# Kernel tuning notes

Measured on AMD Instinct MI355X. Metric: run time of the kernel, lower is better.

Reference implementation:

```python
import jax, jax.numpy as jnp
import numpy as np

VOCAB = 50257
EMB = 256
HID = 256
B = 128
S = 2048


def setup_inputs() -> dict:
    key = jax.random.key(0)
    ks = jax.random.split(key, 18)
    w = 0.05  # weight scale to keep tanh/sigmoid in a sane range
    return {
        "x": jax.random.randint(ks[0], (B,), 0, VOCAB),
        "encoder_states": jax.random.normal(ks[1], (S, B, HID), jnp.float32),
        "hidden": jax.random.normal(ks[2], (1, B, HID), jnp.float32),
        "cell": jax.random.normal(ks[3], (1, B, HID), jnp.float32),
        "emb_table": jax.random.normal(ks[4], (VOCAB, EMB), jnp.float32) * w,
        "W_ih": jax.random.normal(ks[5], (4 * HID, EMB + HID), jnp.float32) * w,
        "W_hh": jax.random.normal(ks[6], (4 * HID, HID), jnp.float32) * w,
        "b_ih": jax.random.normal(ks[7], (4 * HID,), jnp.float32) * w,
        "b_hh": jax.random.normal(ks[8], (4 * HID,), jnp.float32) * w,
        "fc_w": jax.random.normal(ks[9], (VOCAB, HID), jnp.float32) * w,
        "fc_b": jax.random.normal(ks[10], (VOCAB,), jnp.float32) * w,
        "W1_w": jax.random.normal(ks[11], (HID, HID), jnp.float32) * w,
        "W1_b": jax.random.normal(ks[12], (HID,), jnp.float32) * w,
        "W2_w": jax.random.normal(ks[13], (HID, HID), jnp.float32) * w,
        "W2_b": jax.random.normal(ks[14], (HID,), jnp.float32) * w,
        "V_w": jax.random.normal(ks[15], (1, HID), jnp.float32) * w,
        "V_b": jax.random.normal(ks[16], (1,), jnp.float32) * w,
    }


def reference(x, encoder_states, hidden, cell, emb_table, W_ih, W_hh, b_ih, b_hh,
              fc_w, fc_b, W1_w, W1_b, W2_w, W2_b, V_w, V_b):
    # encoder_states: [S, B, H] -> [B, S, H]
    enc = jnp.transpose(encoder_states, (1, 0, 2))
    h0 = hidden[0]  # [B, H]  (num_layers == 1)
    c0 = cell[0]

    # Bahdanau additive attention
    score = jnp.tanh(enc @ W1_w.T + W1_b + (h0 @ W2_w.T + W2_b)[:, None, :])  # [B,S,H]
    attw = jax.nn.softmax(score @ V_w.T + V_b, axis=1)  # [B, S, 1]
    ctx = jnp.sum(attw * enc, axis=1)  # [B, H]

    # embedding (dropout is identity in eval/deterministic mode)
    emb = emb_table[x]  # [B, E]
    rnn_in = jnp.concatenate([ctx, emb], axis=-1)  # [B, H+E]

    # single LSTM step; PyTorch gate order: i, f, g, o
    gates = rnn_in @ W_ih.T + b_ih + h0 @ W_hh.T + b_hh  # [B, 4H]
    i, f, g, o = jnp.split(gates, 4, axis=-1)
    c_new = jax.nn.sigmoid(f) * c0 + jax.nn.sigmoid(i) * jnp.tanh(g)
    h_new = jax.nn.sigmoid(o) * jnp.tanh(c_new)

    predictions = h_new @ fc_w.T + fc_b  # [B, VOCAB]
    return predictions, h_new[None], c_new[None], attw
```

## Files before the change

### kernel.cpp

```cpp
#include <hip/hip_runtime.h>
#include <hip/hip_bf16.h>

#define VOCAB 50257
#define EMB 256
#define HID 256
#define BB 128
#define SS 2048

typedef __attribute__((ext_vector_type(8))) short short8;
typedef __attribute__((ext_vector_type(4))) float f32x4;

__device__ inline unsigned short f2bf(float f) {
    unsigned int u = __float_as_uint(f);
    u += 0x7FFFu + ((u >> 16) & 1u);
    return (unsigned short)(u >> 16);
}
__device__ inline unsigned int pack2(float a, float b) {
    return (unsigned int)f2bf(a) | ((unsigned int)f2bf(b) << 16);
}
__device__ inline uint4 pack8(float4 a, float4 b) {
    return make_uint4(pack2(a.x, a.y), pack2(a.z, a.w), pack2(b.x, b.y), pack2(b.z, b.w));
}

__global__ __launch_bounds__(256) void k_prep(
    const float* __restrict__ hidden, const float* __restrict__ W2,
    const float* __restrict__ W1bias, const float* __restrict__ W2bias,
    const float* __restrict__ W1, unsigned short* __restrict__ W1bf,
    float* __restrict__ qb)
{
    const int bid = blockIdx.x, tid = threadIdx.x;
    if (bid < BB) {
        __shared__ float h0s[HID];
        h0s[tid] = hidden[bid * HID + tid];
        __syncthreads();
        const float4* w2r = (const float4*)(W2 + (size_t)tid * HID);
        float acc = W1bias[tid] + W2bias[tid];
        #pragma unroll 4
        for (int k4 = 0; k4 < HID / 4; ++k4) {
            float4 w = w2r[k4];
            acc += w.x * h0s[k4*4] + w.y * h0s[k4*4+1] + w.z * h0s[k4*4+2] + w.w * h0s[k4*4+3];
        }
        qb[bid * HID + tid] = acc;
    } else {
        int idx = (bid - BB) * 256 + tid;
        float4 v = ((const float4*)W1)[idx];
        ushort4 o;
        o.x = f2bf(v.x); o.y = f2bf(v.y); o.z = f2bf(v.z); o.w = f2bf(v.w);
        ((ushort4*)W1bf)[idx] = o;
    }
}

__global__ __launch_bounds__(256, 2) void k_escore(
    const float* __restrict__ enc, const unsigned short* __restrict__ W1bf,
    const float* __restrict__ qb, const float* __restrict__ Vw,
    const float* __restrict__ Vb, float* __restrict__ e)
{
    __shared__ __align__(16) char As[128 * 64];
    __shared__ __align__(16) char Bs[256 * 64];
    __shared__ float esum[128];

    const int s = blockIdx.x;
    const int tid = threadIdx.x;
    const int lane = tid & 63, wid = tid >> 6;
    const int wm = wid >> 1, wn = wid & 1;
    const int lg = lane >> 4, li = lane & 15;

    if (tid < 128) esum[tid] = 0.f;

    f32x4 acc[4][8];
    #pragma unroll
    for (int m = 0; m < 4; ++m)
        #pragma unroll
        for (int n = 0; n < 8; ++n)
            acc[m][n] = (f32x4){0.f, 0.f, 0.f, 0.f};

    const int arow = tid >> 1, ahalf = tid & 1;
    const float* aptr = enc + ((size_t)s * BB + arow) * HID + ahalf * 16;
    char* awr0 = As + arow * 64 + ((ahalf * 32)      ^ ((arow & 3) << 4));
    char* awr1 = As + arow * 64 + ((ahalf * 32 + 16) ^ ((arow & 3) << 4));
    const int bcol = tid;
    const unsigned short* bptr = W1bf + (size_t)bcol * HID;

    int a_off[4], b_off[8];
    #pragma unroll
    for (int m = 0; m < 4; ++m) { int r = wm*64 + m*16 + li; a_off[m] = r*64 + ((lg*16) ^ ((r&3)<<4)); }
    #pragma unroll
    for (int n = 0; n < 8; ++n) { int c = wn*128 + n*16 + li; b_off[n] = c*64 + ((lg*16) ^ ((c&3)<<4)); }

    for (int kt = 0; kt < 8; ++kt) {
        __syncthreads();
        const float4* ap = (const float4*)(aptr + kt * 32);
        float4 f0 = ap[0], f1 = ap[1], f2 = ap[2], f3 = ap[3];
        *(uint4*)awr0 = pack8(f0, f1);
        *(uint4*)awr1 = pack8(f2, f3);
        const uint4* bp = (const uint4*)(bptr + kt * 32);
        #pragma unroll
        for (int slot = 0; slot < 4; ++slot)
            *(uint4*)(Bs + bcol * 64 + ((slot * 16) ^ ((bcol & 3) << 4))) = bp[slot];
        __syncthreads();
        short8 a[4];
        #pragma unroll
        for (int m = 0; m < 4; ++m) a[m] = *(const short8*)(As + a_off[m]);
        #pragma unroll
        for (int n = 0; n < 8; ++n) {
            short8 b = *(const short8*)(Bs + b_off[n]);
            #pragma unroll
            for (int m = 0; m < 4; ++m)
                acc[m][n] = __builtin_amdgcn_mfma_f32_16x16x32_bf16(a[m], b, acc[m][n], 0, 0, 0);
        }
    }

    #pragma unroll
    for (int m = 0; m < 4; ++m) {
        #pragma unroll
        for (int r = 0; r < 4; ++r) {
            const int brow = wm*64 + m*16 + lg*4 + r;
            float p = 0.f;
            #pragma unroll
            for (int n = 0; n < 8; ++n) {
                const int h = wn*128 + n*16 + li;
                float v = acc[m][n][r] + qb[brow * HID + h];
                p += Vw[h] * tanhf(v);
            }
            p += __shfl_xor(p, 1); p += __shfl_xor(p, 2);
            p += __shfl_xor(p, 4); p += __shfl_xor(p, 8);
            if (li == 0) atomicAdd(&esum[brow], p);
        }
    }
    __syncthreads();
    if (tid < 128) e[(size_t)tid * SS + s] = esum[tid] + Vb[0];
}

__global__ __launch_bounds__(256) void k_softmax(
    const float* __restrict__ e, float* __restrict__ attw)
{
    __shared__ float redm[4];
    __shared__ float reds[4];
    const int b = blockIdx.x, tid = threadIdx.x;
    const float* er = e + (size_t)b * SS;
    float v[8];
    float m = -1e30f;
    #pragma unroll
    for (int i = 0; i < 8; ++i) { v[i] = er[tid + i * 256]; m = fmaxf(m, v[i]); }
    #pragma unroll
    for (int off = 1; off < 64; off <<= 1) m = fmaxf(m, __shfl_xor(m, off));
    if ((tid & 63) == 0) redm[tid >> 6] = m;
    __syncthreads();
    m = fmaxf(fmaxf(redm[0], redm[1]), fmaxf(redm[2], redm[3]));
    float sum = 0.f;
    #pragma unroll
    for (int i = 0; i < 8; ++i) { v[i] = __expf(v[i] - m); sum += v[i]; }
    #pragma unroll
    for (int off = 1; off < 64; off <<= 1) sum += __shfl_xor(sum, off);
    if ((tid & 63) == 0) reds[tid >> 6] = sum;
    __syncthreads();
    const float inv = 1.f / (reds[0] + reds[1] + reds[2] + reds[3]);
    float* aw = attw + (size_t)b * SS;
    #pragma unroll
    for (int i = 0; i < 8; ++i) aw[tid + i * 256] = v[i] * inv;
}

__global__ __launch_bounds__(256) void k_ctx(
    const float* __restrict__ enc, const float* __restrict__ attw,
    float* __restrict__ ctx)
{
    __shared__ float aws[256];
    const int b = blockIdx.x >> 3, chunk = blockIdx.x & 7, tid = threadIdx.x;
    const int s0 = chunk * 256;
    aws[tid] = attw[(size_t)b * SS + s0 + tid];
    __syncthreads();
    float acc = 0.f;
    const float* ep = enc + ((size_t)s0 * BB + b) * HID + tid;
    #pragma unroll 4
    for (int i = 0; i < 256; ++i)
        acc += aws[i] * ep[(size_t)i * BB * HID];
    atomicAdd(&ctx[b * HID + tid], acc);
}

__global__ __launch_bounds__(256) void k_lstm(
    const float* __restrict__ ctx, const int* __restrict__ x,
    const float* __restrict__ emb_table, const float* __restrict__ hidden,
    const float* __restrict__ cell,
    const float* __restrict__ W_ih, const float* __restrict__ W_hh,
    const float* __restrict__ b_ih, const float* __restrict__ b_hh,
    float* __restrict__ out_h, float* __restrict__ out_c)
{
    __shared__ float rin[768];
    __shared__ float gates[1024];
    const int b = blockIdx.x, tid = threadIdx.x;
    rin[tid]       = ctx[b * HID + tid];
    rin[256 + tid] = emb_table[(size_t)x[b] * EMB + tid];
    rin[512 + tid] = hidden[b * HID + tid];
    __syncthreads();
    #pragma unroll
    for (int jj = 0; jj < 4; ++jj) {
        const int j = jj * 256 + tid;
        float acc = b_ih[j] + b_hh[j];
        const float4* wi = (const float4*)(W_ih + (size_t)j * 512);
        #pragma unroll 4
        for (int k4 = 0; k4 < 128; ++k4) {
            float4 w = wi[k4];
            acc += w.x*rin[k4*4] + w.y*rin[k4*4+1] + w.z*rin[k4*4+2] + w.w*rin[k4*4+3];
        }
        const float4* wh = (const float4*)(W_hh + (size_t)j * 256);
        #pragma unroll 4
        for (int k4 = 0; k4 < 64; ++k4) {
            float4 w = wh[k4];
            acc += w.x*rin[512+k4*4] + w.y*rin[512+k4*4+1] + w.z*rin[512+k4*4+2] + w.w*rin[512+k4*4+3];
        }
        gates[j] = acc;
    }
    __syncthreads();
    const float ig = gates[tid], fg = gates[256 + tid];
    const float gg = gates[512 + tid], og = gates[768 + tid];
    const float c0 = cell[b * HID + tid];
    const float si = 1.f / (1.f + __expf(-ig));
    const float sf = 1.f / (1.f + __expf(-fg));
    const float so = 1.f / (1.f + __expf(-og));
    const float cn = sf * c0 + si * tanhf(gg);
    const float hn = so * tanhf(cn);
    out_c[b * HID + tid] = cn;
    out_h[b * HID + tid] = hn;
}

__global__ __launch_bounds__(256, 2) void k_fc(
    const float* __restrict__ hnew, const float* __restrict__ fcw,
    const float* __restrict__ fcb, float* __restrict__ pred)
{
    __shared__ __align__(16) char As[128 * 64];
    __shared__ __align__(16) char Bs[128 * 64];
    const int vbase = blockIdx.x * 128;
    const int tid = threadIdx.x;
    const int lane = tid & 63, wid = tid >> 6;
    const int wm = wid >> 1, wn = wid & 1;
    const int lg = lane >> 4, li = lane & 15;

    f32x4 acc[4][4];
    #pragma unroll
    for (int m = 0; m < 4; ++m)
        #pragma unroll
        for (int n = 0; n < 4; ++n)
            acc[m][n] = (f32x4){0.f, 0.f, 0.f, 0.f};

    const int arow = tid >> 1, ahalf = tid & 1;
    const float* aptr = hnew + (size_t)arow * HID + ahalf * 16;
    char* awr0 = As + arow * 64 + ((ahalf * 32)      ^ ((arow & 3) << 4));
    char* awr1 = As + arow * 64 + ((ahalf * 32 + 16) ^ ((arow & 3) << 4));
    const int bcol = arow;
    const int v = vbase + bcol;
    const bool vok = v < VOCAB;
    const float* bptr = fcw + (size_t)v * HID + ahalf * 16;
    char* bwr0 = Bs + bcol * 64 + ((ahalf * 32)      ^ ((bcol & 3) << 4));
    char* bwr1 = Bs + bcol * 64 + ((ahalf * 32 + 16) ^ ((bcol & 3) << 4));

    int a_off[4], b_off[4];
    #pragma unroll
    for (int m = 0; m < 4; ++m) { int r = wm*64 + m*16 + li; a_off[m] = r*64 + ((lg*16) ^ ((r&3)<<4)); }
    #pragma unroll
    for (int n = 0; n < 4; ++n) { int c = wn*64 + n*16 + li; b_off[n] = c*64 + ((lg*16) ^ ((c&3)<<4)); }

    for (int kt = 0; kt < 8; ++kt) {
        __syncthreads();
        const float4* ap = (const float4*)(aptr + kt * 32);
        float4 f0 = ap[0], f1 = ap[1], f2 = ap[2], f3 = ap[3];
        *(uint4*)awr0 = pack8(f0, f1);
        *(uint4*)awr1 = pack8(f2, f3);
        float4 g0, g1, g2, g3;
        if (vok) {
            const float4* bp = (const float4*)(bptr + kt * 32);
            g0 = bp[0]; g1 = bp[1]; g2 = bp[2]; g3 = bp[3];
        } else {
            g0 = g1 = g2 = g3 = make_float4(0.f, 0.f, 0.f, 0.f);
        }
        *(uint4*)bwr0 = pack8(g0, g1);
        *(uint4*)bwr1 = pack8(g2, g3);
        __syncthreads();
        short8 a[4];
        #pragma unroll
        for (int m = 0; m < 4; ++m) a[m] = *(const short8*)(As + a_off[m]);
        #pragma unroll
        for (int n = 0; n < 4; ++n) {
            short8 b = *(const short8*)(Bs + b_off[n]);
            #pragma unroll
            for (int m = 0; m < 4; ++m)
                acc[m][n] = __builtin_amdgcn_mfma_f32_16x16x32_bf16(a[m], b, acc[m][n], 0, 0, 0);
        }
    }

    #pragma unroll
    for (int m = 0; m < 4; ++m)
        #pragma unroll
        for (int r = 0; r < 4; ++r) {
            const int row = wm*64 + m*16 + lg*4 + r;
            #pragma unroll
            for (int n = 0; n < 4; ++n) {
                const int col = vbase + wn*64 + n*16 + li;
                if (col < VOCAB)
                    pred[(size_t)row * VOCAB + col] = acc[m][n][r] + fcb[col];
            }
        }
}

extern "C" void kernel_launch(void* const* d_in, const int* in_sizes, int n_in,
                              void* d_out, int out_size, void* d_ws, size_t ws_size,
                              hipStream_t stream)
{
    const int*   x      = (const int*)  d_in[0];
    const float* enc    = (const float*)d_in[1];
    const float* hidden = (const float*)d_in[2];
    const float* cell   = (const float*)d_in[3];
    const float* emb    = (const float*)d_in[4];
    const float* W_ih   = (const float*)d_in[5];
    const float* W_hh   = (const float*)d_in[6];
    const float* b_ih   = (const float*)d_in[7];
    const float* b_hh   = (const float*)d_in[8];
    const float* fc_w   = (const float*)d_in[9];
    const float* fc_b   = (const float*)d_in[10];
    const float* W1_w   = (const float*)d_in[11];
    const float* W1_b   = (const float*)d_in[12];
    const float* W2_w   = (const float*)d_in[13];
    const float* W2_b   = (const float*)d_in[14];
    const float* V_w    = (const float*)d_in[15];
    const float* V_b    = (const float*)d_in[16];

    float* out   = (float*)d_out;
    float* pred  = out;
    float* out_h = out + (size_t)BB * VOCAB;
    float* out_c = out_h + BB * HID;
    float* attw  = out_c + BB * HID;

    char* ws = (char*)d_ws;
    unsigned short* W1bf = (unsigned short*)ws;
    float* qb  = (float*)(ws + 131072);
    float* e   = (float*)(ws + 262144);
    float* ctx = (float*)(ws + 262144 + 1048576);

    k_prep   <<<dim3(192),              dim3(256), 0, stream>>>(hidden, W2_w, W1_b, W2_b, W1_w, W1bf, qb);
    k_escore <<<dim3(SS),               dim3(256), 0, stream>>>(enc, W1bf, qb, V_w, V_b, e);
    k_softmax<<<dim3(BB),               dim3(256), 0, stream>>>(e, attw);
    hipMemsetAsync(ctx, 0, BB * HID * sizeof(float), stream);
    k_ctx    <<<dim3(BB * 8),           dim3(256), 0, stream>>>(enc, attw, ctx);
    k_lstm   <<<dim3(BB),               dim3(256), 0, stream>>>(ctx, x, emb, hidden, cell,
                                                                W_ih, W_hh, b_ih, b_hh, out_h, out_c);
    k_fc     <<<dim3((VOCAB + 127)/128), dim3(256), 0, stream>>>(out_h, fc_w, fc_b, pred);
}
```

Before: 766.4 us.

## Enlarge escore tiles to 256 rows with 512 threads, fast tanh, vectorize ctx

The attention score kernel now processes 256 flattened (s,b) rows per block with 512 threads and a K-step of 64, using a wider XOR swizzle. The goal is to amortize W1 tile loads and cut the number of barriers. Tanh is replaced by an exp/rcp approximation to reduce transcendental cost, and V weights are hoisted into registers. The ctx kernel now loads float4 vectors across four s-groups and reduces them in shared memory before the atomics, which improves coalescing. Risks are more register and LDS pressure with 512-thread blocks, plus slightly lower tanh accuracy.

Result: faster. 682.5 us (-10.9%).

```diff
diff --git a/kernel.cpp b/kernel.cpp
--- a/kernel.cpp
+++ b/kernel.cpp
@@ -20,6 +20,11 @@
 }
 __device__ inline uint4 pack8(float4 a, float4 b) {
     return make_uint4(pack2(a.x, a.y), pack2(a.z, a.w), pack2(b.x, b.y), pack2(b.z, b.w));
+}
+__device__ inline float fast_tanh(float x) {
+    x = fminf(fmaxf(x, -9.f), 9.f);
+    float t = __expf(2.f * x);
+    return (t - 1.f) * __builtin_amdgcn_rcpf(t + 1.f);
 }
 
 __global__ __launch_bounds__(256) void k_prep(
@@ -50,22 +55,22 @@
     }
 }
 
-__global__ __launch_bounds__(256, 2) void k_escore(
+__global__ __launch_bounds__(512, 2) void k_escore(
     const float* __restrict__ enc, const unsigned short* __restrict__ W1bf,
     const float* __restrict__ qb, const float* __restrict__ Vw,
     const float* __restrict__ Vb, float* __restrict__ e)
 {
-    __shared__ __align__(16) char As[128 * 64];
-    __shared__ __align__(16) char Bs[256 * 64];
-    __shared__ float esum[128];
-
-    const int s = blockIdx.x;
+    __shared__ __align__(16) char As[256 * 128];
+    __shared__ __align__(16) char Bs[256 * 128];
+    __shared__ float esum[256];
+
     const int tid = threadIdx.x;
     const int lane = tid & 63, wid = tid >> 6;
     const int wm = wid >> 1, wn = wid & 1;
     const int lg = lane >> 4, li = lane & 15;
-
-    if (tid < 128) esum[tid] = 0.f;
+    const size_t row0 = (size_t)blockIdx.x * 256;
+
+    if (tid < 256) esum[tid] = 0.f;
 
     f32x4 acc[4][8];
     #pragma unroll
@@ -74,61 +79,71 @@
         for (int n = 0; n < 8; ++n)
             acc[m][n] = (f32x4){0.f, 0.f, 0.f, 0.f};
 
-    const int arow = tid >> 1, ahalf = tid & 1;
-    const float* aptr = enc + ((size_t)s * BB + arow) * HID + ahalf * 16;
-    char* awr0 = As + arow * 64 + ((ahalf * 32)      ^ ((arow & 3) << 4));
-    char* awr1 = As + arow * 64 + ((ahalf * 32 + 16) ^ ((arow & 3) << 4));
-    const int bcol = tid;
-    const unsigned short* bptr = W1bf + (size_t)bcol * HID;
-
-    int a_off[4], b_off[8];
-    #pragma unroll
-    for (int m = 0; m < 4; ++m) { int r = wm*64 + m*16 + li; a_off[m] = r*64 + ((lg*16) ^ ((r&3)<<4)); }
-    #pragma unroll
-    for (int n = 0; n < 8; ++n) { int c = wn*128 + n*16 + li; b_off[n] = c*64 + ((lg*16) ^ ((c&3)<<4)); }
-
-    for (int kt = 0; kt < 8; ++kt) {
-        __syncthreads();
-        const float4* ap = (const float4*)(aptr + kt * 32);
-        float4 f0 = ap[0], f1 = ap[1], f2 = ap[2], f3 = ap[3];
-        *(uint4*)awr0 = pack8(f0, f1);
-        *(uint4*)awr1 = pack8(f2, f3);
-        const uint4* bp = (const uint4*)(bptr + kt * 32);
-        #pragma unroll
-        for (int slot = 0; slot < 4; ++slot)
-            *(uint4*)(Bs + bcol * 64 + ((slot * 16) ^ ((bcol & 3) << 4))) = bp[slot];
-        __syncthreads();
-        short8 a[4];
-        #pragma unroll
-        for (int m = 0; m < 4; ++m) a[m] = *(const short8*)(As + a_off[m]);
-        #pragma unroll
-        for (int n = 0; n < 8; ++n) {
-            short8 b = *(const short8*)(Bs + b_off[n]);
-            #pragma unroll
-            for (int m = 0; m < 4; ++m)
-                acc[m][n] = __builtin_amdgcn_mfma_f32_16x16x32_bf16(a[m], b, acc[m][n], 0, 0, 0);
-        }
-    }
+    const int a_k16 = tid & 15, a_row0 = tid >> 4;
+    const int b_k8 = tid & 7, b_col0 = tid >> 3;
+
+    for (int kt = 0; kt < 4; ++kt) {
+        __syncthreads();
+        #pragma unroll
+        for (int i = 0; i < 8; ++i) {
+            const int row = a_row0 + 32 * i;
+            float4 v = *((const float4*)(enc + (row0 + row) * HID + kt * 64) + a_k16);
+            uint2 p = make_uint2(pack2(v.x, v.y), pack2(v.z, v.w));
+            *(uint2*)(As + row * 128 + ((a_k16 * 8) ^ ((row & 7) << 4))) = p;
+        }
+        #pragma unroll
+        for (int i = 0; i < 4; ++i) {
+            const int col = b_col0 + 64 * i;
+            uint4 v = *((const uint4*)(W1bf + (size_t)col * HID + kt * 64) + b_k8);
+            *(uint4*)(Bs + col * 128 + ((b_k8 * 16) ^ ((col & 7) << 4))) = v;
+        }
+        __syncthreads();
+        #pragma unroll
+        for (int ks = 0; ks < 2; ++ks) {
+            short8 a[4];
+            #pragma unroll
+            for (int m = 0; m < 4; ++m) {
+                const int r = wm * 64 + m * 16 + li;
+                a[m] = *(const short8*)(As + r * 128 + ((ks * 64 + lg * 16) ^ ((r & 7) << 4)));
+            }
+            #pragma unroll
+            for (int n = 0; n < 8; ++n) {
+                const int c = wn * 128 + n * 16 + li;
+                short8 b = *(const short8*)(Bs + c * 128 + ((ks * 64 + lg * 16) ^ ((c & 7) << 4)));
+                #pragma unroll
+                for (int m = 0; m < 4; ++m)
+                    acc[m][n] = __builtin_amdgcn_mfma_f32_16x16x32_bf16(a[m], b, acc[m][n], 0, 0, 0);
+            }
+        }
+    }
+
+    float vw[8];
+    #pragma unroll
+    for (int n = 0; n < 8; ++n) vw[n] = Vw[wn * 128 + n * 16 + li];
 
     #pragma unroll
     for (int m = 0; m < 4; ++m) {
         #pragma unroll
         for (int r = 0; r < 4; ++r) {
-            const int brow = wm*64 + m*16 + lg*4 + r;
+            const int lrow = wm * 64 + m * 16 + lg * 4 + r;
+            const size_t g = row0 + lrow;
+            const float* qbrow = qb + (size_t)(g & 127) * HID;
             float p = 0.f;
             #pragma unroll
             for (int n = 0; n < 8; ++n) {
-                const int h = wn*128 + n*16 + li;
-                float v = acc[m][n][r] + qb[brow * HID + h];
-                p += Vw[h] * tanhf(v);
+                const int h = wn * 128 + n * 16 + li;
+                p += vw[n] * fast_tanh(acc[m][n][r] + qbrow[h]);
             }
             p += __shfl_xor(p, 1); p += __shfl_xor(p, 2);
             p += __shfl_xor(p, 4); p += __shfl_xor(p, 8);
-            if (li == 0) atomicAdd(&esum[brow], p);
-        }
-    }
-    __syncthreads();
-    if (tid < 128) e[(size_t)tid * SS + s] = esum[tid] + Vb[0];
+            if (li == 0) atomicAdd(&esum[lrow], p);
+        }
+    }
+    __syncthreads();
+    if (tid < 256) {
+        const size_t g = row0 + tid;
+        e[(size_t)(g & 127) * SS + (g >> 7)] = esum[tid] + Vb[0];
+    }
 }
 
 __global__ __launch_bounds__(256) void k_softmax(
@@ -165,16 +180,28 @@
     float* __restrict__ ctx)
 {
     __shared__ float aws[256];
+    __shared__ f32x4 red[256];
     const int b = blockIdx.x >> 3, chunk = blockIdx.x & 7, tid = threadIdx.x;
     const int s0 = chunk * 256;
+    const int hq = tid & 63, sg = tid >> 6;
     aws[tid] = attw[(size_t)b * SS + s0 + tid];
     __syncthreads();
-    float acc = 0.f;
-    const float* ep = enc + ((size_t)s0 * BB + b) * HID + tid;
-    #pragma unroll 4
-    for (int i = 0; i < 256; ++i)
-        acc += aws[i] * ep[(size_t)i * BB * HID];
-    atomicAdd(&ctx[b * HID + tid], acc);
+    const f32x4* base = (const f32x4*)enc + ((size_t)s0 * BB + b) * 64 + hq;
+    f32x4 acc = (f32x4){0.f, 0.f, 0.f, 0.f};
+    #pragma unroll 8
+    for (int i = 0; i < 64; ++i) {
+        const int sl = sg + i * 4;
+        f32x4 v = base[(size_t)sl * (BB * HID / 4)];
+        acc += v * aws[sl];
+    }
+    red[tid] = acc;
+    __syncthreads();
+    if (tid < 64) {
+        f32x4 r = red[tid] + red[tid + 64] + red[tid + 128] + red[tid + 192];
+        #pragma unroll
+        for (int j = 0; j < 4; ++j)
+            atomicAdd(&ctx[b * HID + tid * 4 + j], r[j]);
+    }
 }
 
 __global__ __launch_bounds__(256) void k_lstm(
@@ -335,12 +362,12 @@
     float* e   = (float*)(ws + 262144);
     float* ctx = (float*)(ws + 262144 + 1048576);
 
-    k_prep   <<<dim3(192),              dim3(256), 0, stream>>>(hidden, W2_w, W1_b, W2_b, W1_w, W1bf, qb);
-    k_escore <<<dim3(SS),               dim3(256), 0, stream>>>(enc, W1bf, qb, V_w, V_b, e);
-    k_softmax<<<dim3(BB),               dim3(256), 0, stream>>>(e, attw);
+    k_prep   <<<dim3(192),               dim3(256), 0, stream>>>(hidden, W2_w, W1_b, W2_b, W1_w, W1bf, qb);
+    k_escore <<<dim3(1024),              dim3(512), 0, stream>>>(enc, W1bf, qb, V_w, V_b, e);
+    k_softmax<<<dim3(BB),                dim3(256), 0, stream>>>(e, attw);
     hipMemsetAsync(ctx, 0, BB * HID * sizeof(float), stream);
-    k_ctx    <<<dim3(BB * 8),           dim3(256), 0, stream>>>(enc, attw, ctx);
-    k_lstm   <<<dim3(BB),               dim3(256), 0, stream>>>(ctx, x, emb, hidden, cell,
-                                                                W_ih, W_hh, b_ih, b_hh, out_h, out_c);
+    k_ctx    <<<dim3(BB * 8),            dim3(256), 0, stream>>>(enc, attw, ctx);
+    k_lstm   <<<dim3(BB),                dim3(256), 0, stream>>>(ctx, x, emb, hidden, cell,
+                                                                 W_ih, W_hh, b_ih, b_hh, out_h, out_c);
     k_fc     <<<dim3((VOCAB + 127)/128), dim3(256), 0, stream>>>(out_h, fc_w, fc_b, pred);
 }
```
